# Performance work log

Hardware: AMD Instinct MI355X
Metric: run time of the kernel (lower is better)

The kernel has to match this reference:

```python
import jax, jax.numpy as jnp
import numpy as np

NUM_HEADS = 32


def setup_inputs() -> dict:
    key = jax.random.key(0)
    ks = jax.random.split(key, 6)
    B, S, D = 1, 2048, 4096
    hd = D // NUM_HEADS  # 128
    x = jax.random.normal(ks[0], (B, S, D), dtype=jnp.float32)
    # true rotary frequencies: freqs_cis = exp(i * t * theta^{-2j/hd})
    inv_freq = 1.0 / (10000.0 ** (jnp.arange(0, hd, 2, dtype=jnp.float32) / hd))  # [hd//2]
    angles = jnp.arange(S, dtype=jnp.float32)[:, None] * inv_freq[None, :]  # [S, hd//2]
    freqs_cos = jnp.cos(angles)
    freqs_sin = jnp.sin(angles)
    scale = 0.02
    wq = jax.random.normal(ks[1], (D, D), dtype=jnp.float32) * scale
    wk = jax.random.normal(ks[2], (D, D), dtype=jnp.float32) * scale
    wv = jax.random.normal(ks[3], (D, D), dtype=jnp.float32) * scale
    wo = jax.random.normal(ks[4], (D, D), dtype=jnp.float32) * scale
    return {"x": x, "freqs_cos": freqs_cos, "freqs_sin": freqs_sin,
            "wq": wq, "wk": wk, "wv": wv, "wo": wo}


def _apply_rope(t, cos, sin):
    # t: [B, S, H, hd]; cos/sin: [S, hd//2]
    B, S, H, hd = t.shape
    tr = t.reshape(B, S, H, hd // 2, 2)
    a, b = tr[..., 0], tr[..., 1]
    c = cos[None, :, None, :]
    s = sin[None, :, None, :]
    out_r = a * c - b * s
    out_i = a * s + b * c
    return jnp.stack([out_r, out_i], axis=-1).reshape(B, S, H, hd)


def reference(x, freqs_cos, freqs_sin, wq, wk, wv, wo):
    B, S, D = x.shape
    H = NUM_HEADS
    hd = D // H
    xq = (x @ wq).reshape(B, S, H, hd)
    xk = (x @ wk).reshape(B, S, H, hd)
    xv = (x @ wv).reshape(B, S, H, hd)
    xq = _apply_rope(xq, freqs_cos, freqs_sin)
    xk = _apply_rope(xk, freqs_cos, freqs_sin)
    # [B, H, S, hd]
    xq = xq.transpose(0, 2, 1, 3)
    xk = xk.transpose(0, 2, 1, 3)
    xv = xv.transpose(0, 2, 1, 3)
    scores = jnp.einsum('bhqd,bhkd->bhqk', xq, xk) / jnp.sqrt(jnp.float32(hd))
    scores = jax.nn.softmax(scores.astype(jnp.float32), axis=-1).astype(xq.dtype)
    out = jnp.einsum('bhqk,bhkd->bhqd', scores, xv)
    out = out.transpose(0, 2, 1, 3).reshape(B, S, D)
    return out @ wo
```

## Files before the change

kernel.cpp:

```cpp
#include <hip/hip_runtime.h>
#include <hip/hip_bf16.h>

typedef __hip_bfloat16 bf16;
typedef __attribute__((ext_vector_type(8))) short short8;
typedef __attribute__((ext_vector_type(4))) short short4v;
typedef __attribute__((ext_vector_type(4))) float f32x4;

#define MFMA16(a, b, c) __builtin_amdgcn_mfma_f32_16x16x32_bf16((a), (b), (c), 0, 0, 0)

static __device__ __forceinline__ void gload_lds16(const bf16* g, bf16* l) {
  __builtin_amdgcn_global_load_lds((const __attribute__((address_space(1))) unsigned int*)g,
                                   (__attribute__((address_space(3))) unsigned int*)l,
                                   16, 0, 0);
}

__global__ __launch_bounds__(256) void castx_kernel(const float* __restrict__ x,
                                                    bf16* __restrict__ xb, int n) {
  int i = (blockIdx.x * 256 + threadIdx.x) * 8;
  if (i >= n) return;
  float4 v0 = *(const float4*)(x + i);
  float4 v1 = *(const float4*)(x + i + 4);
  bf16 tmp[8];
  tmp[0] = __float2bfloat16(v0.x); tmp[1] = __float2bfloat16(v0.y);
  tmp[2] = __float2bfloat16(v0.z); tmp[3] = __float2bfloat16(v0.w);
  tmp[4] = __float2bfloat16(v1.x); tmp[5] = __float2bfloat16(v1.y);
  tmp[6] = __float2bfloat16(v1.z); tmp[7] = __float2bfloat16(v1.w);
  *(short8*)(xb + i) = *(short8*)tmp;
}

__global__ __launch_bounds__(256) void tw_kernel(const float* __restrict__ W,
                                                 bf16* __restrict__ WT) {
  __shared__ bf16 tile[64][65];
  int b = blockIdx.x;
  int tk = (b >> 6) * 64;
  int tn = (b & 63) * 64;
  int t = threadIdx.x;
  int c = t & 63, r0 = t >> 6;
#pragma unroll
  for (int i = 0; i < 16; ++i) {
    int r = i * 4 + r0;
    tile[c][r] = __float2bfloat16(W[(size_t)(tk + r) * 4096 + tn + c]);
  }
  __syncthreads();
#pragma unroll
  for (int i = 0; i < 16; ++i) {
    int r = i * 4 + r0;
    WT[(size_t)(tn + r) * 4096 + tk + c] = tile[r][c];
  }
}

__global__ __launch_bounds__(512) void gemmQK8(const bf16* __restrict__ A,
                                               const bf16* __restrict__ Bt,
                                               bf16* __restrict__ Qb,
                                               bf16* __restrict__ Kb,
                                               const float* __restrict__ fcos,
                                               const float* __restrict__ fsin) {
  __shared__ bf16 LDS[2 * 32768];
  const int K = 4096, NK = 64;
  int g = blockIdx.x;
  int xcd = g & 7, loc = g >> 3;
  int bm = (xcd >> 2) * 4 + (loc >> 3);
  int bn = (xcd & 3) * 8 + (loc & 7);
  int t = threadIdx.x, lane = t & 63, w = t >> 6;
  int wm = w >> 2, wn = w & 3;
  int lr = lane & 15, lg = lane >> 4;
  int rsw = (lr >> 1) & 3;
  f32x4 acc[8][4] = {};

  const bf16* Ab = A + (size_t)bm * 256 * K;
  const bf16* Bb = Bt + (size_t)bn * 256 * K;
  int sr4 = t >> 2;
  int sg = (t & 3) ^ ((t >> 3) & 3);

#define SA(nb, kt2, kh)                                                          \
  do {                                                                           \
    _Pragma("unroll") for (int j = 0; j < 2; ++j)                                \
      gload_lds16(Ab + (size_t)(j * 128 + sr4) * K + (kt2) * 64 + (kh) * 32 + sg * 8, \
                  LDS + (nb) + (kh) * 8192 + (j * 512 + t) * 8);                 \
  } while (0)
#define SB(nb, kt2, kh)                                                          \
  do {                                                                           \
    _Pragma("unroll") for (int j = 0; j < 2; ++j)                                \
      gload_lds16(Bb + (size_t)(j * 128 + sr4) * K + (kt2) * 64 + (kh) * 32 + sg * 8, \
                  LDS + (nb) + 16384 + (kh) * 8192 + (j * 512 + t) * 8);         \
  } while (0)
#define AFR(base, kc, mi) \
  (*(const short8*)(LDS + (base) + (kc) * 8192 + (wm * 128 + (mi) * 16 + lr) * 32 + ((lg ^ rsw) << 3)))
#define BFR(base, kc, nf) \
  (*(const short8*)(LDS + (base) + 16384 + (kc) * 8192 + (wn * 64 + (nf) * 16 + lr) * 32 + ((lg ^ rsw) << 3)))

  SA(0, 0, 0); SB(0, 0, 0); SA(0, 0, 1); SB(0, 0, 1);
  asm volatile("s_waitcnt vmcnt(4)" ::: "memory");
  __builtin_amdgcn_s_barrier();

  int cur = 0;
  for (int kt = 0; kt < NK; ++kt) {
    int base = cur * 32768;
    int nbf = (cur ^ 1) * 32768;
    bool pf = (kt + 1) < NK;
    short8 a[4], b[4];

#pragma unroll
    for (int nf = 0; nf < 4; ++nf) b[nf] = BFR(base, 0, nf);
#pragma unroll
    for (int i = 0; i < 4; ++i) a[i] = AFR(base, 0, i);
    if (pf) SA(nbf, kt + 1, 0);
    __builtin_amdgcn_s_setprio(1);
#pragma unroll
    for (int i = 0; i < 4; ++i)
#pragma unroll
      for (int nf = 0; nf < 4; ++nf)
        acc[i][nf] = MFMA16(a[i], b[nf], acc[i][nf]);
    __builtin_amdgcn_s_setprio(0);
#pragma unroll
    for (int i = 0; i < 4; ++i) a[i] = AFR(base, 0, 4 + i);
    if (pf) SB(nbf, kt + 1, 0);
    __builtin_amdgcn_s_setprio(1);
#pragma unroll
    for (int i = 0; i < 4; ++i)
#pragma unroll
      for (int nf = 0; nf < 4; ++nf)
        acc[4 + i][nf] = MFMA16(a[i], b[nf], acc[4 + i][nf]);
    __builtin_amdgcn_s_setprio(0);
    if (pf)
      asm volatile("s_waitcnt vmcnt(4)" ::: "memory");
    else
      asm volatile("s_waitcnt vmcnt(0)" ::: "memory");
    __builtin_amdgcn_s_barrier();

#pragma unroll
    for (int nf = 0; nf < 4; ++nf) b[nf] = BFR(base, 1, nf);
#pragma unroll
    for (int i = 0; i < 4; ++i) a[i] = AFR(base, 1, i);
    if (pf) SA(nbf, kt + 1, 1);
    __builtin_amdgcn_s_setprio(1);
#pragma unroll
    for (int i = 0; i < 4; ++i)
#pragma unroll
      for (int nf = 0; nf < 4; ++nf)
        acc[i][nf] = MFMA16(a[i], b[nf], acc[i][nf]);
    __builtin_amdgcn_s_setprio(0);
#pragma unroll
    for (int i = 0; i < 4; ++i) a[i] = AFR(base, 1, 4 + i);
    if (pf) SB(nbf, kt + 1, 1);
    __builtin_amdgcn_s_setprio(1);
#pragma unroll
    for (int i = 0; i < 4; ++i)
#pragma unroll
      for (int nf = 0; nf < 4; ++nf)
        acc[4 + i][nf] = MFMA16(a[i], b[nf], acc[4 + i][nf]);
    __builtin_amdgcn_s_setprio(0);
    asm volatile("s_waitcnt vmcnt(4)" ::: "memory");
    __builtin_amdgcn_s_barrier();

    cur ^= 1;
  }
#undef SA
#undef SB
#undef AFR
#undef BFR

  int sect = bn >> 4, bnl = bn & 15;
  bf16* Cb = sect ? Kb : Qb;
  const float qs = sect ? 1.0f : 0.08838834764831845f;
#pragma unroll
  for (int mi = 0; mi < 8; ++mi)
#pragma unroll
    for (int nf = 0; nf < 4; ++nf) {
      int col = bnl * 256 + wn * 64 + nf * 16 + lr;
      int row0 = bm * 256 + wm * 128 + mi * 16 + lg * 4;
      int ip = (col >> 1) & 63;
      float sgn = (col & 1) ? 1.0f : -1.0f;
#pragma unroll
      for (int r = 0; r < 4; ++r) {
        int row = row0 + r;
        float mine = acc[mi][nf][r];
        float oth = __shfl_xor(mine, 1);
        float cv = fcos[row * 64 + ip];
        float sv = fsin[row * 64 + ip];
        float v = (mine * cv + sgn * oth * sv) * qs;
        Cb[(size_t)row * 4096 + col] = __float2bfloat16(v);
      }
    }
}

template <int EPI>
__global__ __launch_bounds__(512) void gemmB(const bf16* __restrict__ A,
                                             const bf16* __restrict__ Bt,
                                             void* __restrict__ Cv,
                                             int M, int N) {
  __shared__ bf16 LDS[2 * 24576];
  const int K = 4096, NK = 64;
  int g = blockIdx.x;
  int xcd = g & 7, loc = g >> 3;
  int bm = (xcd >> 1) * 4 + (loc >> 3);
  int bn = (xcd & 1) * 8 + (loc & 7);
  int t = threadIdx.x, lane = t & 63, w = t >> 6;
  int lr = lane & 15, lg = lane >> 4;
  int rsw = (lr >> 1) & 3;
  f32x4 acc[8][2] = {};

  const bf16* Ab = A + (size_t)bm * 128 * K;
  const bf16* Bb = Bt + (size_t)bn * 256 * K;
  int sr4 = t >> 2;
  int sg = (t & 3) ^ ((t >> 3) & 3);

#define SAB(nb, kt2, kh)                                                         \
  gload_lds16(Ab + (size_t)sr4 * K + (kt2) * 64 + (kh) * 32 + sg * 8,            \
              LDS + (nb) + (kh) * 4096 + t * 8)
#define SBB(nb, kt2, kh)                                                         \
  do {                                                                           \
    _Pragma("unroll") for (int j = 0; j < 2; ++j)                                \
      gload_lds16(Bb + (size_t)(j * 128 + sr4) * K + (kt2) * 64 + (kh) * 32 + sg * 8, \
                  LDS + (nb) + 8192 + (kh) * 8192 + (j * 512 + t) * 8);          \
  } while (0)
#define AFRB(base, kc, mi) \
  (*(const short8*)(LDS + (base) + (kc) * 4096 + ((mi) * 16 + lr) * 32 + ((lg ^ rsw) << 3)))
#define BFRB(base, kc, nf) \
  (*(const short8*)(LDS + (base) + 8192 + (kc) * 8192 + (w * 32 + (nf) * 16 + lr) * 32 + ((lg ^ rsw) << 3)))

  SAB(0, 0, 0); SBB(0, 0, 0); SAB(0, 0, 1); SBB(0, 0, 1);
  asm volatile("s_waitcnt vmcnt(3)" ::: "memory");
  __builtin_amdgcn_s_barrier();

  int cur = 0;
  for (int kt = 0; kt < NK; ++kt) {
    int base = cur * 24576;
    int nbf = (cur ^ 1) * 24576;
    bool pf = (kt + 1) < NK;
    short8 a[8], b[2];

    b[0] = BFRB(base, 0, 0); b[1] = BFRB(base, 0, 1);
#pragma unroll
    for (int i = 0; i < 8; ++i) a[i] = AFRB(base, 0, i);
    if (pf) { SAB(nbf, kt + 1, 0); SBB(nbf, kt + 1, 0); }
    if (pf)
      asm volatile("s_waitcnt vmcnt(3)" ::: "memory");
    else
      asm volatile("s_waitcnt vmcnt(0)" ::: "memory");
    __builtin_amdgcn_s_barrier();
    __builtin_amdgcn_s_setprio(1);
#pragma unroll
    for (int i = 0; i < 8; ++i)
#pragma unroll
      for (int nf = 0; nf < 2; ++nf)
        acc[i][nf] = MFMA16(a[i], b[nf], acc[i][nf]);
    __builtin_amdgcn_s_setprio(0);

    b[0] = BFRB(base, 1, 0); b[1] = BFRB(base, 1, 1);
#pragma unroll
    for (int i = 0; i < 8; ++i) a[i] = AFRB(base, 1, i);
    if (pf) { SAB(nbf, kt + 1, 1); SBB(nbf, kt + 1, 1); }
    asm volatile("s_waitcnt vmcnt(3)" ::: "memory");
    __builtin_amdgcn_s_barrier();
    __builtin_amdgcn_s_setprio(1);
#pragma unroll
    for (int i = 0; i < 8; ++i)
#pragma unroll
      for (int nf = 0; nf < 2; ++nf)
        acc[i][nf] = MFMA16(a[i], b[nf], acc[i][nf]);
    __builtin_amdgcn_s_setprio(0);

    cur ^= 1;
  }
#undef SAB
#undef SBB
#undef AFRB
#undef BFRB

#pragma unroll
  for (int mi = 0; mi < 8; ++mi)
#pragma unroll
    for (int nf = 0; nf < 2; ++nf) {
      int col = bn * 256 + w * 32 + nf * 16 + lr;
      int row0 = bm * 128 + mi * 16 + lg * 4;
      if constexpr (EPI == 3) {
        bf16 tmp[4];
#pragma unroll
        for (int r = 0; r < 4; ++r) tmp[r] = __float2bfloat16(acc[mi][nf][r]);
        *(short4v*)((bf16*)Cv + (size_t)col * M + row0) = *(short4v*)tmp;
      } else {
#pragma unroll
        for (int r = 0; r < 4; ++r)
          ((float*)Cv)[(size_t)(row0 + r) * N + col] = acc[mi][nf][r];
      }
    }
}

__global__ __launch_bounds__(512, 2) void attn_fwd(const bf16* __restrict__ Q,
                                                   const bf16* __restrict__ K,
                                                   const bf16* __restrict__ Vt,
                                                   bf16* __restrict__ O) {
  __shared__ bf16 Kbuf[2][64 * 128];
  __shared__ bf16 Vbuf[2][128 * 64];
  __shared__ char Ps_all[8][2][2048];
  const int S = 2048, D = 4096, HD = 128, NT = 32;
  int g = blockIdx.y * 8 + blockIdx.x;
  int wid = (g & 7) * 32 + (g >> 3);
  int h = wid >> 3, qb = wid & 7;
  int tid = threadIdx.x, lane = tid & 63, w = tid >> 6;
  int lr = lane & 15, lg = lane >> 4;
  int q0 = qb * 256 + w * 32;
  int swz = (lr & 7) << 4;

  const bf16* Kh = K + h * HD;
  const bf16* Vh = Vt + (size_t)h * HD * S;

  short8 aq[2][4];
#pragma unroll
  for (int u = 0; u < 2; ++u)
#pragma unroll
    for (int c = 0; c < 4; ++c)
      aq[u][c] = *(const short8*)(Q + (size_t)(q0 + u * 16 + lr) * D + h * HD + c * 32 + lg * 8);

  int kr = lane >> 4, ksl = lane & 15;
  int vr = lane >> 3, vsl = lane & 7;

  f32x4 accO[2][8] = {};
  float lsum[2] = {0.f, 0.f};

#define STAGE(b, ttile)                                                            \
  do {                                                                             \
    int kv0_ = (ttile) * 64;                                                       \
    _Pragma("unroll") for (int ii = 0; ii < 2; ++ii) {                             \
      int row = w * 8 + ii * 4 + kr;                                               \
      gload_lds16(Kh + (size_t)(kv0_ + row) * D + ((ksl ^ (row & 7)) << 3),        \
                  &Kbuf[b][(w * 8 + ii * 4) * 128]);                               \
    }                                                                              \
    _Pragma("unroll") for (int ii = 0; ii < 2; ++ii) {                             \
      int row = w * 16 + ii * 8 + vr;                                              \
      gload_lds16(Vh + (size_t)row * S + kv0_ + ((vsl ^ (row & 7)) << 3),          \
                  &Vbuf[b][(w * 16 + ii * 8) * 64]);                               \
    }                                                                              \
  } while (0)

  int cur = 0;
  STAGE(0, 0);
  for (int tt = 0; tt < NT; ++tt) {
    if (tt + 1 < NT) {
      STAGE(cur ^ 1, tt + 1);
      asm volatile("s_waitcnt vmcnt(4)" ::: "memory");
    } else {
      asm volatile("s_waitcnt vmcnt(0)" ::: "memory");
    }
    __builtin_amdgcn_s_barrier();
    const bf16* Kb_ = Kbuf[cur];
    const bf16* Vb_ = Vbuf[cur];

    f32x4 sf[2][4] = {};
#pragma unroll
    for (int j = 0; j < 4; ++j)
#pragma unroll
      for (int c = 0; c < 4; ++c) {
        short8 kf = *(const short8*)(Kb_ + (j * 16 + lr) * 128 +
                                     (((c * 4 + lg) ^ (lr & 7)) << 3));
        sf[0][j] = MFMA16(kf, aq[0][c], sf[0][j]);
        sf[1][j] = MFMA16(kf, aq[1][c], sf[1][j]);
      }
#pragma unroll
    for (int u = 0; u < 2; ++u) {
      char* Ps = Ps_all[w][u];
#pragma unroll
      for (int j = 0; j < 4; ++j) {
        float p0 = __expf(sf[u][j][0]);
        float p1 = __expf(sf[u][j][1]);
        float p2 = __expf(sf[u][j][2]);
        float p3 = __expf(sf[u][j][3]);
        lsum[u] += (p0 + p1) + (p2 + p3);
        bf16 pk[4] = {__float2bfloat16(p0), __float2bfloat16(p1),
                      __float2bfloat16(p2), __float2bfloat16(p3)};
        *(short4v*)(Ps + lr * 128 + ((j * 32 + lg * 8) ^ swz)) = *(short4v*)pk;
      }
    }
#pragma unroll
    for (int t2 = 0; t2 < 2; ++t2) {
      short8 pa0 = *(const short8*)(Ps_all[w][0] + lr * 128 + ((t2 * 64 + lg * 16) ^ swz));
      short8 pa1 = *(const short8*)(Ps_all[w][1] + lr * 128 + ((t2 * 64 + lg * 16) ^ swz));
#pragma unroll
      for (int n = 0; n < 8; ++n) {
        short8 bv = *(const short8*)(Vb_ + (n * 16 + lr) * 64 +
                                     (((t2 * 4 + lg) ^ (lr & 7)) << 3));
        accO[0][n] = MFMA16(pa0, bv, accO[0][n]);
        accO[1][n] = MFMA16(pa1, bv, accO[1][n]);
      }
    }
    __builtin_amdgcn_s_barrier();
    cur ^= 1;
  }
#undef STAGE

#pragma unroll
  for (int u = 0; u < 2; ++u) {
    float ls = lsum[u];
    ls += __shfl_xor(ls, 16);
    ls += __shfl_xor(ls, 32);
    float rs[4];
#pragma unroll
    for (int r = 0; r < 4; ++r)
      rs[r] = 1.f / __shfl(ls, lg * 4 + r);
#pragma unroll
    for (int n = 0; n < 8; ++n)
#pragma unroll
      for (int r = 0; r < 4; ++r) {
        int row = q0 + u * 16 + lg * 4 + r;
        int col = h * HD + n * 16 + lr;
        O[(size_t)row * D + col] = __float2bfloat16(accO[u][n][r] * rs[r]);
      }
  }
}

extern "C" void kernel_launch(void* const* d_in, const int* in_sizes, int n_in,
                              void* d_out, int out_size, void* d_ws, size_t ws_size,
                              hipStream_t stream) {
  const float* x    = (const float*)d_in[0];
  const float* fcos = (const float*)d_in[1];
  const float* fsin = (const float*)d_in[2];
  const float* wq   = (const float*)d_in[3];
  const float* wk   = (const float*)d_in[4];
  const float* wv   = (const float*)d_in[5];
  const float* wo   = (const float*)d_in[6];
  float* out = (float*)d_out;

  const int S = 2048, D = 4096;
  const size_t MB = 1024 * 1024;
  char* ws = (char*)d_ws;
  bf16* xb  = (bf16*)(ws);
  bf16* wT2 = (bf16*)(ws + 16 * MB);
  bf16* Vt  = (bf16*)(ws + 48 * MB);
  bf16* Qb  = (bf16*)(ws + 80 * MB);
  bf16* Kb  = (bf16*)(ws + 96 * MB);
  bf16* AO  = (bf16*)(ws);

  int n = S * D;
  castx_kernel<<<n / (256 * 8), 256, 0, stream>>>(x, xb, n);

  tw_kernel<<<4096, 256, 0, stream>>>(wq, wT2);
  tw_kernel<<<4096, 256, 0, stream>>>(wk, wT2 + (size_t)4096 * 4096);
  gemmQK8<<<256, 512, 0, stream>>>(xb, wT2, Qb, Kb, fcos, fsin);

  tw_kernel<<<4096, 256, 0, stream>>>(wv, wT2);
  gemmB<3><<<256, 512, 0, stream>>>(xb, wT2, Vt, S, D);

  attn_fwd<<<dim3(8, 32), 512, 0, stream>>>(Qb, Kb, Vt, AO);

  tw_kernel<<<4096, 256, 0, stream>>>(wo, wT2);
  gemmB<4><<<256, 512, 0, stream>>>(AO, wT2, out, S, D);
}
```

Measured before the change: 410.0 us.

## Load GEMM weight fragments directly from global into registers, bypassing LDS

In the QK and B projection GEMMs, the B (transposed weight) tile is no longer staged through LDS. Each wave loads its MFMA fragments directly from global memory into registers, double-buffered one half-k-step ahead. This cuts LDS footprint, LDS traffic and barrier-related stalls for B. The trade-off is uncoalesced, row-strided global loads, duplicate loads across waves sharing columns, and reliance on cache hits and correct vmcnt accounting.

```diff
diff --git a/kernel.cpp b/kernel.cpp
--- a/kernel.cpp
+++ b/kernel.cpp
@@ -49,13 +49,13 @@
   }
 }
 
-__global__ __launch_bounds__(512) void gemmQK8(const bf16* __restrict__ A,
+__global__ __launch_bounds__(512) void gemmQK9(const bf16* __restrict__ A,
                                                const bf16* __restrict__ Bt,
                                                bf16* __restrict__ Qb,
                                                bf16* __restrict__ Kb,
                                                const float* __restrict__ fcos,
                                                const float* __restrict__ fsin) {
-  __shared__ bf16 LDS[2 * 32768];
+  __shared__ bf16 LDS[2 * 16384];
   const int K = 4096, NK = 64;
   int g = blockIdx.x;
   int xcd = g & 7, loc = g >> 3;
@@ -72,93 +72,96 @@
   int sr4 = t >> 2;
   int sg = (t & 3) ^ ((t >> 3) & 3);
 
+  const bf16* brow[4];
+#pragma unroll
+  for (int nf = 0; nf < 4; ++nf)
+    brow[nf] = Bb + (size_t)(wn * 64 + nf * 16 + lr) * K + lg * 8;
+
 #define SA(nb, kt2, kh)                                                          \
   do {                                                                           \
     _Pragma("unroll") for (int j = 0; j < 2; ++j)                                \
       gload_lds16(Ab + (size_t)(j * 128 + sr4) * K + (kt2) * 64 + (kh) * 32 + sg * 8, \
                   LDS + (nb) + (kh) * 8192 + (j * 512 + t) * 8);                 \
   } while (0)
-#define SB(nb, kt2, kh)                                                          \
-  do {                                                                           \
-    _Pragma("unroll") for (int j = 0; j < 2; ++j)                                \
-      gload_lds16(Bb + (size_t)(j * 128 + sr4) * K + (kt2) * 64 + (kh) * 32 + sg * 8, \
-                  LDS + (nb) + 16384 + (kh) * 8192 + (j * 512 + t) * 8);         \
-  } while (0)
 #define AFR(base, kc, mi) \
   (*(const short8*)(LDS + (base) + (kc) * 8192 + (wm * 128 + (mi) * 16 + lr) * 32 + ((lg ^ rsw) << 3)))
-#define BFR(base, kc, nf) \
-  (*(const short8*)(LDS + (base) + 16384 + (kc) * 8192 + (wn * 64 + (nf) * 16 + lr) * 32 + ((lg ^ rsw) << 3)))
-
-  SA(0, 0, 0); SB(0, 0, 0); SA(0, 0, 1); SB(0, 0, 1);
-  asm volatile("s_waitcnt vmcnt(4)" ::: "memory");
+
+  short8 b0[4], b1[4];
+  SA(0, 0, 0); SA(0, 0, 1);
+#pragma unroll
+  for (int nf = 0; nf < 4; ++nf) b0[nf] = *(const short8*)(brow[nf]);
+  asm volatile("s_waitcnt vmcnt(6)" ::: "memory");
   __builtin_amdgcn_s_barrier();
 
   int cur = 0;
   for (int kt = 0; kt < NK; ++kt) {
-    int base = cur * 32768;
-    int nbf = (cur ^ 1) * 32768;
+    int base = cur * 16384;
+    int nbf = (cur ^ 1) * 16384;
     bool pf = (kt + 1) < NK;
-    short8 a[4], b[4];
-
-#pragma unroll
-    for (int nf = 0; nf < 4; ++nf) b[nf] = BFR(base, 0, nf);
-#pragma unroll
-    for (int i = 0; i < 4; ++i) a[i] = AFR(base, 0, i);
+
+#pragma unroll
+    for (int nf = 0; nf < 4; ++nf)
+      b1[nf] = *(const short8*)(brow[nf] + kt * 64 + 32);
     if (pf) SA(nbf, kt + 1, 0);
-    __builtin_amdgcn_s_setprio(1);
-#pragma unroll
-    for (int i = 0; i < 4; ++i)
-#pragma unroll
-      for (int nf = 0; nf < 4; ++nf)
-        acc[i][nf] = MFMA16(a[i], b[nf], acc[i][nf]);
-    __builtin_amdgcn_s_setprio(0);
-#pragma unroll
-    for (int i = 0; i < 4; ++i) a[i] = AFR(base, 0, 4 + i);
-    if (pf) SB(nbf, kt + 1, 0);
-    __builtin_amdgcn_s_setprio(1);
-#pragma unroll
-    for (int i = 0; i < 4; ++i)
-#pragma unroll
-      for (int nf = 0; nf < 4; ++nf)
-        acc[4 + i][nf] = MFMA16(a[i], b[nf], acc[4 + i][nf]);
-    __builtin_amdgcn_s_setprio(0);
-    if (pf)
-      asm volatile("s_waitcnt vmcnt(4)" ::: "memory");
-    else
-      asm volatile("s_waitcnt vmcnt(0)" ::: "memory");
-    __builtin_amdgcn_s_barrier();
-
-#pragma unroll
-    for (int nf = 0; nf < 4; ++nf) b[nf] = BFR(base, 1, nf);
-#pragma unroll
-    for (int i = 0; i < 4; ++i) a[i] = AFR(base, 1, i);
+    {
+      short8 a[4];
+#pragma unroll
+      for (int i = 0; i < 4; ++i) a[i] = AFR(base, 0, i);
+      __builtin_amdgcn_s_setprio(1);
+#pragma unroll
+      for (int i = 0; i < 4; ++i)
+#pragma unroll
+        for (int nf = 0; nf < 4; ++nf)
+          acc[i][nf] = MFMA16(a[i], b0[nf], acc[i][nf]);
+      __builtin_amdgcn_s_setprio(0);
+#pragma unroll
+      for (int i = 0; i < 4; ++i) a[i] = AFR(base, 0, 4 + i);
+      __builtin_amdgcn_s_setprio(1);
+#pragma unroll
+      for (int i = 0; i < 4; ++i)
+#pragma unroll
+        for (int nf = 0; nf < 4; ++nf)
+          acc[4 + i][nf] = MFMA16(a[i], b0[nf], acc[4 + i][nf]);
+      __builtin_amdgcn_s_setprio(0);
+    }
+    __builtin_amdgcn_sched_barrier(0);
+    asm volatile("s_waitcnt vmcnt(6)" ::: "memory");
+    __builtin_amdgcn_s_barrier();
+
+    int ktn = pf ? kt + 1 : kt;
+#pragma unroll
+    for (int nf = 0; nf < 4; ++nf)
+      b0[nf] = *(const short8*)(brow[nf] + ktn * 64);
     if (pf) SA(nbf, kt + 1, 1);
-    __builtin_amdgcn_s_setprio(1);
-#pragma unroll
-    for (int i = 0; i < 4; ++i)
-#pragma unroll
-      for (int nf = 0; nf < 4; ++nf)
-        acc[i][nf] = MFMA16(a[i], b[nf], acc[i][nf]);
-    __builtin_amdgcn_s_setprio(0);
-#pragma unroll
-    for (int i = 0; i < 4; ++i) a[i] = AFR(base, 1, 4 + i);
-    if (pf) SB(nbf, kt + 1, 1);
-    __builtin_amdgcn_s_setprio(1);
-#pragma unroll
-    for (int i = 0; i < 4; ++i)
-#pragma unroll
-      for (int nf = 0; nf < 4; ++nf)
-        acc[4 + i][nf] = MFMA16(a[i], b[nf], acc[4 + i][nf]);
-    __builtin_amdgcn_s_setprio(0);
-    asm volatile("s_waitcnt vmcnt(4)" ::: "memory");
+    {
+      short8 a[4];
+#pragma unroll
+      for (int i = 0; i < 4; ++i) a[i] = AFR(base, 1, i);
+      __builtin_amdgcn_s_setprio(1);
+#pragma unroll
+      for (int i = 0; i < 4; ++i)
+#pragma unroll
+        for (int nf = 0; nf < 4; ++nf)
+          acc[i][nf] = MFMA16(a[i], b1[nf], acc[i][nf]);
+      __builtin_amdgcn_s_setprio(0);
+#pragma unroll
+      for (int i = 0; i < 4; ++i) a[i] = AFR(base, 1, 4 + i);
+      __builtin_amdgcn_s_setprio(1);
+#pragma unroll
+      for (int i = 0; i < 4; ++i)
+#pragma unroll
+        for (int nf = 0; nf < 4; ++nf)
+          acc[4 + i][nf] = MFMA16(a[i], b1[nf], acc[4 + i][nf]);
+      __builtin_amdgcn_s_setprio(0);
+    }
+    __builtin_amdgcn_sched_barrier(0);
+    asm volatile("s_waitcnt vmcnt(6)" ::: "memory");
     __builtin_amdgcn_s_barrier();
 
     cur ^= 1;
   }
 #undef SA
-#undef SB
 #undef AFR
-#undef BFR
 
   int sect = bn >> 4, bnl = bn & 15;
   bf16* Cb = sect ? Kb : Qb;
@@ -185,11 +188,11 @@
 }
 
 template <int EPI>
-__global__ __launch_bounds__(512) void gemmB(const bf16* __restrict__ A,
-                                             const bf16* __restrict__ Bt,
-                                             void* __restrict__ Cv,
-                                             int M, int N) {
-  __shared__ bf16 LDS[2 * 24576];
+__global__ __launch_bounds__(512) void gemmB2(const bf16* __restrict__ A,
+                                              const bf16* __restrict__ Bt,
+                                              void* __restrict__ Cv,
+                                              int M, int N) {
+  __shared__ bf16 LDS[2 * 8192];
   const int K = 4096, NK = 64;
   int g = blockIdx.x;
   int xcd = g & 7, loc = g >> 3;
@@ -205,68 +208,93 @@
   int sr4 = t >> 2;
   int sg = (t & 3) ^ ((t >> 3) & 3);
 
+  const bf16* brow[2];
+#pragma unroll
+  for (int nf = 0; nf < 2; ++nf)
+    brow[nf] = Bb + (size_t)(w * 32 + nf * 16 + lr) * K + lg * 8;
+
 #define SAB(nb, kt2, kh)                                                         \
   gload_lds16(Ab + (size_t)sr4 * K + (kt2) * 64 + (kh) * 32 + sg * 8,            \
               LDS + (nb) + (kh) * 4096 + t * 8)
-#define SBB(nb, kt2, kh)                                                         \
-  do {                                                                           \
-    _Pragma("unroll") for (int j = 0; j < 2; ++j)                                \
-      gload_lds16(Bb + (size_t)(j * 128 + sr4) * K + (kt2) * 64 + (kh) * 32 + sg * 8, \
-                  LDS + (nb) + 8192 + (kh) * 8192 + (j * 512 + t) * 8);          \
-  } while (0)
 #define AFRB(base, kc, mi) \
   (*(const short8*)(LDS + (base) + (kc) * 4096 + ((mi) * 16 + lr) * 32 + ((lg ^ rsw) << 3)))
-#define BFRB(base, kc, nf) \
-  (*(const short8*)(LDS + (base) + 8192 + (kc) * 8192 + (w * 32 + (nf) * 16 + lr) * 32 + ((lg ^ rsw) << 3)))
-
-  SAB(0, 0, 0); SBB(0, 0, 0); SAB(0, 0, 1); SBB(0, 0, 1);
+
+  short8 b0[2], b1[2];
+  SAB(0, 0, 0); SAB(0, 0, 1);
+#pragma unroll
+  for (int nf = 0; nf < 2; ++nf) b0[nf] = *(const short8*)(brow[nf]);
   asm volatile("s_waitcnt vmcnt(3)" ::: "memory");
   __builtin_amdgcn_s_barrier();
 
   int cur = 0;
   for (int kt = 0; kt < NK; ++kt) {
-    int base = cur * 24576;
-    int nbf = (cur ^ 1) * 24576;
+    int base = cur * 8192;
+    int nbf = (cur ^ 1) * 8192;
     bool pf = (kt + 1) < NK;
-    short8 a[8], b[2];
-
-    b[0] = BFRB(base, 0, 0); b[1] = BFRB(base, 0, 1);
-#pragma unroll
-    for (int i = 0; i < 8; ++i) a[i] = AFRB(base, 0, i);
-    if (pf) { SAB(nbf, kt + 1, 0); SBB(nbf, kt + 1, 0); }
-    if (pf)
-      asm volatile("s_waitcnt vmcnt(3)" ::: "memory");
-    else
-      asm volatile("s_waitcnt vmcnt(0)" ::: "memory");
-    __builtin_amdgcn_s_barrier();
-    __builtin_amdgcn_s_setprio(1);
-#pragma unroll
-    for (int i = 0; i < 8; ++i)
-#pragma unroll
-      for (int nf = 0; nf < 2; ++nf)
-        acc[i][nf] = MFMA16(a[i], b[nf], acc[i][nf]);
-    __builtin_amdgcn_s_setprio(0);
-
-    b[0] = BFRB(base, 1, 0); b[1] = BFRB(base, 1, 1);
-#pragma unroll
-    for (int i = 0; i < 8; ++i) a[i] = AFRB(base, 1, i);
-    if (pf) { SAB(nbf, kt + 1, 1); SBB(nbf, kt + 1, 1); }
+
+#pragma unroll
+    for (int nf = 0; nf < 2; ++nf)
+      b1[nf] = *(const short8*)(brow[nf] + kt * 64 + 32);
+    if (pf) SAB(nbf, kt + 1, 0);
+    {
+      short8 a[4];
+#pragma unroll
+      for (int i = 0; i < 4; ++i) a[i] = AFRB(base, 0, i);
+      __builtin_amdgcn_s_setprio(1);
+#pragma unroll
+      for (int i = 0; i < 4; ++i)
+#pragma unroll
+        for (int nf = 0; nf < 2; ++nf)
+          acc[i][nf] = MFMA16(a[i], b0[nf], acc[i][nf]);
+      __builtin_amdgcn_s_setprio(0);
+#pragma unroll
+      for (int i = 0; i < 4; ++i) a[i] = AFRB(base, 0, 4 + i);
+      __builtin_amdgcn_s_setprio(1);
+#pragma unroll
+      for (int i = 0; i < 4; ++i)
+#pragma unroll
+        for (int nf = 0; nf < 2; ++nf)
+          acc[4 + i][nf] = MFMA16(a[i], b0[nf], acc[4 + i][nf]);
+      __builtin_amdgcn_s_setprio(0);
+    }
+    __builtin_amdgcn_sched_barrier(0);
     asm volatile("s_waitcnt vmcnt(3)" ::: "memory");
     __builtin_amdgcn_s_barrier();
-    __builtin_amdgcn_s_setprio(1);
-#pragma unroll
-    for (int i = 0; i < 8; ++i)
-#pragma unroll
-      for (int nf = 0; nf < 2; ++nf)
-        acc[i][nf] = MFMA16(a[i], b[nf], acc[i][nf]);
-    __builtin_amdgcn_s_setprio(0);
+
+    int ktn = pf ? kt + 1 : kt;
+#pragma unroll
+    for (int nf = 0; nf < 2; ++nf)
+      b0[nf] = *(const short8*)(brow[nf] + ktn * 64);
+    if (pf) SAB(nbf, kt + 1, 1);
+    {
+      short8 a[4];
+#pragma unroll
+      for (int i = 0; i < 4; ++i) a[i] = AFRB(base, 1, i);
+      __builtin_amdgcn_s_setprio(1);
+#pragma unroll
+      for (int i = 0; i < 4; ++i)
+#pragma unroll
+        for (int nf = 0; nf < 2; ++nf)
+          acc[i][nf] = MFMA16(a[i], b1[nf], acc[i][nf]);
+      __builtin_amdgcn_s_setprio(0);
+#pragma unroll
+      for (int i = 0; i < 4; ++i) a[i] = AFRB(base, 1, 4 + i);
+      __builtin_amdgcn_s_setprio(1);
+#pragma unroll
+      for (int i = 0; i < 4; ++i)
+#pragma unroll
+        for (int nf = 0; nf < 2; ++nf)
+          acc[4 + i][nf] = MFMA16(a[i], b1[nf], acc[4 + i][nf]);
+      __builtin_amdgcn_s_setprio(0);
+    }
+    __builtin_amdgcn_sched_barrier(0);
+    asm volatile("s_waitcnt vmcnt(3)" ::: "memory");
+    __builtin_amdgcn_s_barrier();
 
     cur ^= 1;
   }
 #undef SAB
-#undef SBB
 #undef AFRB
-#undef BFRB
 
 #pragma unroll
   for (int mi = 0; mi < 8; ++mi)
@@ -436,13 +464,13 @@
 
   tw_kernel<<<4096, 256, 0, stream>>>(wq, wT2);
   tw_kernel<<<4096, 256, 0, stream>>>(wk, wT2 + (size_t)4096 * 4096);
-  gemmQK8<<<256, 512, 0, stream>>>(xb, wT2, Qb, Kb, fcos, fsin);
+  gemmQK9<<<256, 512, 0, stream>>>(xb, wT2, Qb, Kb, fcos, fsin);
 
   tw_kernel<<<4096, 256, 0, stream>>>(wv, wT2);
-  gemmB<3><<<256, 512, 0, stream>>>(xb, wT2, Vt, S, D);
+  gemmB2<3><<<256, 512, 0, stream>>>(xb, wT2, Vt, S, D);
 
   attn_fwd<<<dim3(8, 32), 512, 0, stream>>>(Qb, Kb, Vt, AO);
 
   tw_kernel<<<4096, 256, 0, stream>>>(wo, wT2);
-  gemmB<4><<<256, 512, 0, stream>>>(AO, wT2, out, S, D);
-}
+  gemmB2<4><<<256, 512, 0, stream>>>(AO, wT2, out, S, D);
+}
```

Result: slower. 538.4 us (+31.3%).

## Merge x cast and Wq/Wk transposes into one launch; raise MFMA wave priority

Applied to the files above, without the earlier changes.

Replaces the x-to-bf16 cast kernel and the two weight transpose launches with one 2D-grid kernel that picks its task by blockIdx.y. This removes launch overhead and the gaps between three small kernels. Separately, the attention kernel raises wave priority with s_setprio around the QK and PV MFMA loops so matrix work is favoured over exp/softmax on other waves. The x-cast blocks do little work next to the transpose blocks, so load balance inside the merged grid is uneven.

```diff
diff --git a/kernel.cpp b/kernel.cpp
--- a/kernel.cpp
+++ b/kernel.cpp
@@ -14,18 +14,42 @@
                                    16, 0, 0);
 }
 
-__global__ __launch_bounds__(256) void castx_kernel(const float* __restrict__ x,
-                                                    bf16* __restrict__ xb, int n) {
-  int i = (blockIdx.x * 256 + threadIdx.x) * 8;
-  if (i >= n) return;
-  float4 v0 = *(const float4*)(x + i);
-  float4 v1 = *(const float4*)(x + i + 4);
-  bf16 tmp[8];
-  tmp[0] = __float2bfloat16(v0.x); tmp[1] = __float2bfloat16(v0.y);
-  tmp[2] = __float2bfloat16(v0.z); tmp[3] = __float2bfloat16(v0.w);
-  tmp[4] = __float2bfloat16(v1.x); tmp[5] = __float2bfloat16(v1.y);
-  tmp[6] = __float2bfloat16(v1.z); tmp[7] = __float2bfloat16(v1.w);
-  *(short8*)(xb + i) = *(short8*)tmp;
+__global__ __launch_bounds__(256) void prep3_kernel(const float* __restrict__ x,
+                                                    bf16* __restrict__ xb,
+                                                    const float* __restrict__ wq,
+                                                    const float* __restrict__ wk,
+                                                    bf16* __restrict__ wT2) {
+  if (blockIdx.y == 2) {
+    int i = (blockIdx.x * 256 + threadIdx.x) * 8;
+    float4 v0 = *(const float4*)(x + i);
+    float4 v1 = *(const float4*)(x + i + 4);
+    bf16 tmp[8];
+    tmp[0] = __float2bfloat16(v0.x); tmp[1] = __float2bfloat16(v0.y);
+    tmp[2] = __float2bfloat16(v0.z); tmp[3] = __float2bfloat16(v0.w);
+    tmp[4] = __float2bfloat16(v1.x); tmp[5] = __float2bfloat16(v1.y);
+    tmp[6] = __float2bfloat16(v1.z); tmp[7] = __float2bfloat16(v1.w);
+    *(short8*)(xb + i) = *(short8*)tmp;
+    return;
+  }
+  const float* W = blockIdx.y ? wk : wq;
+  bf16* WT = wT2 + (blockIdx.y ? (size_t)4096 * 4096 : 0);
+  __shared__ bf16 tile[64][65];
+  int b = blockIdx.x;
+  int tk = (b >> 6) * 64;
+  int tn = (b & 63) * 64;
+  int t = threadIdx.x;
+  int c = t & 63, r0 = t >> 6;
+#pragma unroll
+  for (int i = 0; i < 16; ++i) {
+    int r = i * 4 + r0;
+    tile[c][r] = __float2bfloat16(W[(size_t)(tk + r) * 4096 + tn + c]);
+  }
+  __syncthreads();
+#pragma unroll
+  for (int i = 0; i < 16; ++i) {
+    int r = i * 4 + r0;
+    WT[(size_t)(tn + r) * 4096 + tk + c] = tile[r][c];
+  }
 }
 
 __global__ __launch_bounds__(256) void tw_kernel(const float* __restrict__ W,
@@ -348,6 +372,7 @@
     const bf16* Vb_ = Vbuf[cur];
 
     f32x4 sf[2][4] = {};
+    __builtin_amdgcn_s_setprio(1);
 #pragma unroll
     for (int j = 0; j < 4; ++j)
 #pragma unroll
@@ -357,6 +382,7 @@
         sf[0][j] = MFMA16(kf, aq[0][c], sf[0][j]);
         sf[1][j] = MFMA16(kf, aq[1][c], sf[1][j]);
       }
+    __builtin_amdgcn_s_setprio(0);
 #pragma unroll
     for (int u = 0; u < 2; ++u) {
       char* Ps = Ps_all[w][u];
@@ -376,6 +402,7 @@
     for (int t2 = 0; t2 < 2; ++t2) {
       short8 pa0 = *(const short8*)(Ps_all[w][0] + lr * 128 + ((t2 * 64 + lg * 16) ^ swz));
       short8 pa1 = *(const short8*)(Ps_all[w][1] + lr * 128 + ((t2 * 64 + lg * 16) ^ swz));
+      __builtin_amdgcn_s_setprio(1);
 #pragma unroll
       for (int n = 0; n < 8; ++n) {
         short8 bv = *(const short8*)(Vb_ + (n * 16 + lr) * 64 +
@@ -383,6 +410,7 @@
         accO[0][n] = MFMA16(pa0, bv, accO[0][n]);
         accO[1][n] = MFMA16(pa1, bv, accO[1][n]);
       }
+      __builtin_amdgcn_s_setprio(0);
     }
     __builtin_amdgcn_s_barrier();
     cur ^= 1;
@@ -431,11 +459,7 @@
   bf16* Kb  = (bf16*)(ws + 96 * MB);
   bf16* AO  = (bf16*)(ws);
 
-  int n = S * D;
-  castx_kernel<<<n / (256 * 8), 256, 0, stream>>>(x, xb, n);
-
-  tw_kernel<<<4096, 256, 0, stream>>>(wq, wT2);
-  tw_kernel<<<4096, 256, 0, stream>>>(wk, wT2 + (size_t)4096 * 4096);
+  prep3_kernel<<<dim3(4096, 3), 256, 0, stream>>>(x, xb, wq, wk, wT2);
   gemmQK8<<<256, 512, 0, stream>>>(xb, wT2, Qb, Kb, fcos, fsin);
 
   tw_kernel<<<4096, 256, 0, stream>>>(wv, wT2);
```

Result: no change. 406.5 us (-0.8%).
